# Kernel tuning notes

Hardware: AMD Instinct MI355X
Metric: run time of the kernel (lower is better)

The kernel has to match this reference:

```python
import jax, jax.numpy as jnp
import numpy as np

D = 768      # num_hiddens (hardcoded by dense1/dense2/ln in the source)
H = 12       # num_heads
NEG = -1000000.0
EPS = 1e-5


def setup_inputs() -> dict:
    key = jax.random.key(0)
    ks = jax.random.split(key, 14)
    B, Lq, Lk = 8, 1024, 1024
    s = 0.02
    return {
        "queries": jax.random.normal(ks[0], (B, Lq, D), dtype=jnp.float32),
        "keys":    jax.random.normal(ks[1], (B, Lk, D), dtype=jnp.float32),
        "values":  jax.random.normal(ks[2], (B, Lk, D), dtype=jnp.float32),
        # binary padding masks; count_nonzero along axis 1 gives valid lens
        "mask_1": jax.random.randint(ks[3], (B, Lk), 0, 2, dtype=jnp.int32),
        "mask_2": jax.random.randint(ks[4], (B, Lq), 0, 2, dtype=jnp.int32),
        # projection weights stored as [in, out] (torch Linear is y = x @ W.T)
        "Wq": jax.random.normal(ks[5], (D, D), dtype=jnp.float32) * s,
        "Wk": jax.random.normal(ks[6], (D, D), dtype=jnp.float32) * s,
        "Wv": jax.random.normal(ks[7], (D, D), dtype=jnp.float32) * s,
        "Wo": jax.random.normal(ks[8], (D, D), dtype=jnp.float32) * s,
        "d1_w": jax.random.normal(ks[9], (D, D), dtype=jnp.float32) * s,
        "d1_b": jnp.zeros((D,), dtype=jnp.float32),
        "d2_w": jax.random.normal(ks[10], (D, D), dtype=jnp.float32) * s,
        "d2_b": jnp.zeros((D,), dtype=jnp.float32),
        "ln_g": jnp.ones((D,), dtype=jnp.float32),
        "ln_b": jnp.zeros((D,), dtype=jnp.float32),
    }


def _cross_att(queries, keys, values, mask_1, mask_2,
               Wq, Wk, Wv, Wo, d1_w, d1_b, d2_w, d2_b, ln_g, ln_b):
    B, Lq, _ = queries.shape
    Lk = keys.shape[1]
    hd = D // H
    # project + split heads: [B, H, L, hd]
    q = (queries @ Wq).reshape(B, Lq, H, hd).transpose(0, 2, 1, 3)
    k = (keys    @ Wk).reshape(B, Lk, H, hd).transpose(0, 2, 1, 3)
    v = (values  @ Wv).reshape(B, Lk, H, hd).transpose(0, 2, 1, 3)
    scores = jnp.einsum('bhqd,bhkd->bhqk', q, k) / jnp.sqrt(jnp.float32(hd))
    # dual-axis prefix mask from nonzero counts
    vl1 = jnp.sum(mask_1 != 0, axis=1)  # [B], masks key axis
    vl2 = jnp.sum(mask_2 != 0, axis=1)  # [B], masks query axis
    col_ok = jnp.arange(Lk)[None, None, None, :] < vl1[:, None, None, None]
    row_ok = jnp.arange(Lq)[None, None, :, None] < vl2[:, None, None, None]
    scores = jnp.where(col_ok & row_ok, scores, NEG)
    attn = jax.nn.softmax(scores, axis=-1)
    out = jnp.einsum('bhqk,bhkd->bhqd', attn, v)
    out = out.transpose(0, 2, 1, 3).reshape(B, Lq, D)
    mha = out @ Wo
    ffn = jax.nn.relu(mha @ d1_w + d1_b) @ d2_w + d2_b
    x = ffn + mha  # dropout is identity in eval
    mu = jnp.mean(x, axis=-1, keepdims=True)
    var = jnp.mean(jnp.square(x - mu), axis=-1, keepdims=True)
    return (x - mu) / jnp.sqrt(var + EPS) * ln_g + ln_b


def reference(queries, keys, values, mask_1, mask_2,
              Wq, Wk, Wv, Wo, d1_w, d1_b, d2_w, d2_b, ln_g, ln_b):
    return _cross_att(queries, keys, values, mask_1, mask_2,
                      Wq, Wk, Wv, Wo, d1_w, d1_b, d2_w, d2_b, ln_g, ln_b)
```

## Files before the change

### kernel.cpp

```cpp
#include <hip/hip_runtime.h>
#include <hip/hip_bf16.h>
#include <type_traits>

#define DM   768
#define NH   12
#define HD   64
#define BATCH 8
#define SEQ  1024
#define NROWS (BATCH * SEQ)

typedef short bf16x8 __attribute__((ext_vector_type(8)));
typedef float f32x4 __attribute__((ext_vector_type(4)));

__device__ inline unsigned short f2b(float x) {
    union { float f; unsigned int u; } v; v.f = x;
    return (unsigned short)((v.u + 0x8000u) >> 16);
}
__device__ inline unsigned int f2b2(float lo, float hi) {
    union { float f; unsigned int u; } a, b; a.f = lo; b.f = hi;
    return __builtin_amdgcn_perm(b.u + 0x8000u, a.u + 0x8000u, 0x07060302u);
}
__device__ inline float b2f(unsigned short u) {
    union { float f; unsigned int x; } v; v.x = ((unsigned int)u) << 16;
    return v.f;
}

__device__ inline void gld16(const unsigned short* g, unsigned short* l) {
    __builtin_amdgcn_global_load_lds(
        (const __attribute__((address_space(1))) unsigned int*)g,
        (__attribute__((address_space(3))) unsigned int*)l, 16, 0, 0);
}

__device__ __forceinline__ void mm_loop(const unsigned short* __restrict__ A,
                                        const unsigned short* __restrict__ Wt,
                                        int m0, int n0, int t,
                                        unsigned short (*As)[128][32],
                                        unsigned short (*Ws)[128][32],
                                        f32x4 (&acc)[4][4]) {
    const int w = t >> 6, lane = t & 63;
    const int quad = lane >> 4, l16 = lane & 15;
    const int wm = w & 1, wn = w >> 1;
    const int srow = 16 * w + (lane >> 2);
    const int scol = 8 * ((lane & 3) ^ ((lane >> 3) & 3));
    const int swr = (quad ^ ((l16 >> 1) & 3)) * 8;

#pragma unroll
    for (int i = 0; i < 4; ++i)
#pragma unroll
        for (int j = 0; j < 4; ++j) acc[i][j] = (f32x4){0.f, 0.f, 0.f, 0.f};

    const unsigned short* aP = &A[(size_t)(m0 + srow) * DM + scol];
    const unsigned short* wP = &Wt[(size_t)(n0 + srow) * DM + scol];

    auto stage = [&](int kk, int b) {
#pragma unroll
        for (int j = 0; j < 2; ++j) {
            gld16(aP + (size_t)(64 * j) * DM + kk * 32, &As[b][16 * w + 64 * j][0]);
            gld16(wP + (size_t)(64 * j) * DM + kk * 32, &Ws[b][16 * w + 64 * j][0]);
        }
    };
    auto compute = [&](int b) {
        bf16x8 av[4], bv[4];
#pragma unroll
        for (int i = 0; i < 4; ++i)
            av[i] = *(const bf16x8*)&As[b][wm * 64 + 16 * i + l16][swr];
#pragma unroll
        for (int i = 0; i < 4; ++i)
            bv[i] = *(const bf16x8*)&Ws[b][wn * 64 + 16 * i + l16][swr];
#pragma unroll
        for (int i = 0; i < 4; ++i)
#pragma unroll
            for (int j = 0; j < 4; ++j)
                acc[i][j] = __builtin_amdgcn_mfma_f32_16x16x32_bf16(bv[j], av[i], acc[i][j], 0, 0, 0);
    };

    stage(0, 0);
    stage(1, 1);
    int b = 0;
#pragma unroll 1
    for (int k = 0; k < 22; ++k) {
        int nb = b + 2; if (nb >= 3) nb -= 3;
        stage(k + 2, nb);
        asm volatile("s_waitcnt vmcnt(8)" ::: "memory");
        __builtin_amdgcn_s_barrier();
        compute(b);
        asm volatile("" ::: "memory");
        __builtin_amdgcn_s_barrier();
        if (++b == 3) b = 0;
    }
    asm volatile("s_waitcnt vmcnt(4)" ::: "memory");
    __builtin_amdgcn_s_barrier();
    compute(b);
    asm volatile("" ::: "memory");
    __builtin_amdgcn_s_barrier();
    if (++b == 3) b = 0;
    asm volatile("s_waitcnt vmcnt(0)" ::: "memory");
    __builtin_amdgcn_s_barrier();
    compute(b);
}

__global__ __launch_bounds__(256) void prep_kernel(const float* __restrict__ w0,
                                                   const float* __restrict__ w1,
                                                   const float* __restrict__ w2,
                                                   const float* __restrict__ w3,
                                                   const float* __restrict__ w4,
                                                   const float* __restrict__ w5,
                                                   unsigned short* __restrict__ wt,
                                                   unsigned short* __restrict__ wob,
                                                   const float* __restrict__ qin,
                                                   const float* __restrict__ kin,
                                                   const float* __restrict__ vin,
                                                   unsigned short* __restrict__ oq,
                                                   unsigned short* __restrict__ ok,
                                                   unsigned short* __restrict__ ov) {
    const int z = blockIdx.z;
    const int t = threadIdx.x;

    if (z >= 6) {
        const int linear = (z - 6) * 576 + blockIdx.y * 24 + blockIdx.x;
        const int c0 = linear * 2;
        const int g = c0 / 3072;
        const int r = c0 % 3072;
        const float* src = (g == 0) ? qin : (g == 1) ? kin : vin;
        unsigned short* dst = (g == 0) ? oq : (g == 1) ? ok : ov;
        const size_t i = ((size_t)r * 256 + t) * 8;
        float4 f0 = ((const float4*)(src + i))[0];
        float4 f1 = ((const float4*)(src + i))[1];
        float4 f2 = ((const float4*)(src + i + 2048))[0];
        float4 f3 = ((const float4*)(src + i + 2048))[1];
        uint4 p;
        p.x = f2b2(f0.x, f0.y); p.y = f2b2(f0.z, f0.w);
        p.z = f2b2(f1.x, f1.y); p.w = f2b2(f1.z, f1.w);
        *(uint4*)(dst + i) = p;
        p.x = f2b2(f2.x, f2.y); p.y = f2b2(f2.z, f2.w);
        p.z = f2b2(f3.x, f3.y); p.w = f2b2(f3.z, f3.w);
        *(uint4*)(dst + i + 2048) = p;
        return;
    }

    {
        __shared__ float tile[32][33];
        const float* W = (z == 0) ? w0 : (z == 1) ? w1 : (z == 2) ? w2
                       : (z == 3) ? w3 : (z == 4) ? w4 : w5;
        unsigned short* Wt = wt + (size_t)z * DM * DM;
        const int n0 = blockIdx.x * 32;
        const int k0 = blockIdx.y * 32;
        const int tx = t & 31;
        const int ty = t >> 5;
        float v[4];
#pragma unroll
        for (int r = 0; r < 4; ++r) {
            v[r] = W[(size_t)(k0 + ty + 8 * r) * DM + n0 + tx];
            tile[ty + 8 * r][tx] = v[r];
        }
        if (z == 3) {
#pragma unroll
            for (int r = 0; r < 4; ++r)
                wob[(size_t)(k0 + ty + 8 * r) * DM + n0 + tx] = f2b(v[r]);
        }
        __syncthreads();
#pragma unroll
        for (int r = 0; r < 4; ++r)
            Wt[(size_t)(n0 + ty + 8 * r) * DM + k0 + tx] = f2b(tile[tx][ty + 8 * r]);
    }
}

__global__ __launch_bounds__(256) void qkv_gemm(const unsigned short* __restrict__ aq,
                                                const unsigned short* __restrict__ akk,
                                                const unsigned short* __restrict__ av_,
                                                unsigned short* __restrict__ wt,
                                                const unsigned short* __restrict__ wob,
                                                unsigned short* __restrict__ c0,
                                                unsigned short* __restrict__ c1,
                                                unsigned short* __restrict__ c2,
                                                const int* __restrict__ m1,
                                                const int* __restrict__ m2,
                                                int* __restrict__ lens) {
    __shared__ __align__(16) unsigned short As[3][128][32];
    __shared__ __align__(16) unsigned short Ws[3][128][32];

    const int t = threadIdx.x;
    const size_t WT = (size_t)DM * DM;

    const unsigned short* A;
    const unsigned short* Wop;
    unsigned short* C;
    float cs;
    int m0, n0;

    if (blockIdx.y == 0) {
        if (blockIdx.x >= 52) return;
        if (blockIdx.x >= 36) {
            const int bid = blockIdx.x - 36;
            int* redi = (int*)&As[0][0][0];
            const int b = bid & 7;
            const int* m = (bid < 8) ? m1 : m2;
            int cnt = 0;
            for (int i = t; i < SEQ; i += 256) cnt += (m[b * SEQ + i] != 0) ? 1 : 0;
            redi[t] = cnt;
            __syncthreads();
            for (int off = 128; off > 0; off >>= 1) {
                if (t < off) redi[t] += redi[t + off];
                __syncthreads();
            }
            if (t == 0) lens[bid] = redi[0];
            return;
        }
        A = wt + 4 * WT;
        Wop = wob;
        C = wt + 6 * WT;
        cs = 1.0f;
        m0 = (blockIdx.x % 6) * 128;
        n0 = (blockIdx.x / 6) * 128;
    } else {
        const int yy = blockIdx.y - 1;
        const int g = yy / 6;
        m0 = blockIdx.x * 128;
        n0 = (yy % 6) * 128;
        A = (g == 0) ? aq : (g == 1) ? akk : av_;
        Wop = wt + (size_t)g * WT;
        C = (g == 0) ? c0 : (g == 1) ? c1 : c2;
        cs = (g == 0) ? 0.18033688f : 1.0f;
    }

    f32x4 acc[4][4];
    mm_loop(A, Wop, m0, n0, t, As, Ws, acc);

    const int w = t >> 6, lane = t & 63;
    const int quad = lane >> 4, l16 = lane & 15;
    const int wm = w & 1, wn = w >> 1;

#pragma unroll
    for (int i = 0; i < 4; ++i) {
        const int tok = m0 + wm * 64 + 16 * i + l16;
        unsigned short* crow = &C[(size_t)tok * DM + n0 + wn * 64 + quad * 4];
#pragma unroll
        for (int j = 0; j < 4; ++j) {
            uint2 pr;
            pr.x = f2b2(acc[i][j][0] * cs, acc[i][j][1] * cs);
            pr.y = f2b2(acc[i][j][2] * cs, acc[i][j][3] * cs);
            *(uint2*)(crow + 16 * j) = pr;
        }
    }
}

__global__ __launch_bounds__(256) void vpart_kernel(const unsigned short* __restrict__ v,
                                                    float* __restrict__ vp) {
    __shared__ float red[4][64];
    const int t = threadIdx.x;
    const int bh = blockIdx.x;
    const int chunk = blockIdx.y;
    const int b = bh / NH, h = bh % NH;
    const int d = t & 63, rg = t >> 6;
    const unsigned short* base =
        v + (size_t)(b * SEQ + chunk * 128 + rg * 32) * DM + h * HD + d;
    float s = 0.0f;
#pragma unroll 4
    for (int i = 0; i < 32; ++i) s += b2f(base[(size_t)i * DM]);
    red[rg][d] = s;
    __syncthreads();
    if (rg == 0)
        vp[((size_t)bh * 8 + chunk) * 64 + d] = red[0][d] + red[1][d] + red[2][d] + red[3][d];
}

template <typename CT>
__global__ __launch_bounds__(256) void gemm_bf(const unsigned short* __restrict__ A,
                                               const unsigned short* __restrict__ Wt,
                                               CT* __restrict__ C,
                                               const float* __restrict__ bias,
                                               const unsigned short* __restrict__ res,
                                               int relu) {
    __shared__ __align__(16) unsigned short As[3][128][32];
    __shared__ __align__(16) unsigned short Ws[3][128][32];

    const int t = threadIdx.x;
    const int m0 = blockIdx.x * 128;
    const int n0 = blockIdx.y * 128;

    f32x4 acc[4][4];
    mm_loop(A, Wt, m0, n0, t, As, Ws, acc);

    const int w = t >> 6, lane = t & 63;
    const int quad = lane >> 4, l16 = lane & 15;
    const int wm = w & 1, wn = w >> 1;

#pragma unroll
    for (int i = 0; i < 4; ++i) {
        const int tok = m0 + wm * 64 + 16 * i + l16;
#pragma unroll
        for (int j = 0; j < 4; ++j) {
            const int fb = n0 + wn * 64 + 16 * j + quad * 4;
            float cv0 = acc[i][j][0], cv1 = acc[i][j][1];
            float cv2 = acc[i][j][2], cv3 = acc[i][j][3];
            if (bias) {
                const float4 bb = *(const float4*)&bias[fb];
                cv0 += bb.x; cv1 += bb.y; cv2 += bb.z; cv3 += bb.w;
            }
            if (relu) {
                cv0 = fmaxf(cv0, 0.0f); cv1 = fmaxf(cv1, 0.0f);
                cv2 = fmaxf(cv2, 0.0f); cv3 = fmaxf(cv3, 0.0f);
            }
            if (res) {
                const uint2 rr = *(const uint2*)&res[(size_t)tok * DM + fb];
                cv0 += b2f((unsigned short)(rr.x & 0xffffu));
                cv1 += b2f((unsigned short)(rr.x >> 16));
                cv2 += b2f((unsigned short)(rr.y & 0xffffu));
                cv3 += b2f((unsigned short)(rr.y >> 16));
            }
            if constexpr (std::is_same<CT, float>::value) {
                float4 o4; o4.x = cv0; o4.y = cv1; o4.z = cv2; o4.w = cv3;
                *(float4*)&C[(size_t)tok * DM + fb] = o4;
            } else {
                uint2 pr;
                pr.x = f2b2(cv0, cv1);
                pr.y = f2b2(cv2, cv3);
                *(uint2*)&C[(size_t)tok * DM + fb] = pr;
            }
        }
    }
}

__global__ __launch_bounds__(256) void gemm_mh(const unsigned short* __restrict__ A,
                                               const unsigned short* __restrict__ wt,
                                               unsigned short* __restrict__ cm,
                                               unsigned short* __restrict__ ch,
                                               const float* __restrict__ d1b) {
    __shared__ __align__(16) unsigned short As[3][128][32];
    __shared__ __align__(16) unsigned short Ws[3][128][32];

    const int t = threadIdx.x;
    const int unit = blockIdx.y / 6;
    const unsigned short* Wt = wt + (size_t)(unit ? 6 : 3) * DM * DM;
    unsigned short* C = unit ? ch : cm;
    const int m0 = blockIdx.x * 128;
    const int n0 = (blockIdx.y % 6) * 128;

    f32x4 acc[4][4];
    mm_loop(A, Wt, m0, n0, t, As, Ws, acc);

    const int w = t >> 6, lane = t & 63;
    const int quad = lane >> 4, l16 = lane & 15;
    const int wm = w & 1, wn = w >> 1;

#pragma unroll
    for (int i = 0; i < 4; ++i) {
        const int tok = m0 + wm * 64 + 16 * i + l16;
#pragma unroll
        for (int j = 0; j < 4; ++j) {
            const int fb = n0 + wn * 64 + 16 * j + quad * 4;
            float cv0 = acc[i][j][0], cv1 = acc[i][j][1];
            float cv2 = acc[i][j][2], cv3 = acc[i][j][3];
            if (unit) {
                const float4 bb = *(const float4*)&d1b[fb];
                cv0 = fmaxf(cv0 + bb.x, 0.0f);
                cv1 = fmaxf(cv1 + bb.y, 0.0f);
                cv2 = fmaxf(cv2 + bb.z, 0.0f);
                cv3 = fmaxf(cv3 + bb.w, 0.0f);
            }
            uint2 pr;
            pr.x = f2b2(cv0, cv1);
            pr.y = f2b2(cv2, cv3);
            *(uint2*)&C[(size_t)tok * DM + fb] = pr;
        }
    }
}

__global__ __launch_bounds__(256) void attn_mfma(const unsigned short* Q,
                                                 const unsigned short* __restrict__ K,
                                                 const unsigned short* __restrict__ V,
                                                 unsigned short* O,
                                                 const int* __restrict__ lens,
                                                 const float* __restrict__ vp) {
    __shared__ __align__(16) unsigned short Ks[64][72];
    __shared__ __align__(16) unsigned short Vt[64][72];
    __shared__ __align__(16) unsigned short Ps[4][16][72];

    const int t = threadIdx.x;
    const int bid = blockIdx.x;
    const int q0 = (bid & 15) * 64;
    const int h = (bid >> 4) % NH;
    const int b = bid / (16 * NH);
    const int vl1 = lens[b];
    const int vl2 = lens[8 + b];
    const int wid = t >> 6;
    const int lane = t & 63;
    const int quad = lane >> 4;
    const int l16 = lane & 15;
    const size_t vpb = (size_t)(b * NH + h) * 8 * 64;

    if (q0 >= vl2 || vl1 == 0) {
        float vm[4];
#pragma unroll
        for (int ct = 0; ct < 4; ++ct) {
            float s = 0.0f;
#pragma unroll
            for (int c = 0; c < 8; ++c) s += vp[vpb + (size_t)c * 64 + 16 * ct + l16];
            vm[ct] = s * (1.0f / 1024.0f);
        }
#pragma unroll
        for (int r = 0; r < 4; ++r) {
            const size_t row = (size_t)(b * SEQ + q0 + 16 * wid + quad * 4 + r);
#pragma unroll
            for (int ct = 0; ct < 4; ++ct)
                O[row * DM + h * HD + 16 * ct + l16] = f2b(vm[ct]);
        }
        return;
    }

    bf16x8 qa0, qa1;
    {
        const unsigned short* qp =
            &Q[(size_t)(b * SEQ + q0 + 16 * wid + l16) * DM + h * HD + quad * 8];
        qa0 = *(const bf16x8*)qp;
        qa1 = *(const bf16x8*)(qp + 32);
    }

    f32x4 o[4];
#pragma unroll
    for (int ct = 0; ct < 4; ++ct) o[ct] = (f32x4){0.f, 0.f, 0.f, 0.f};
    float suml[4];
    bool rbad[4];
#pragma unroll
    for (int r = 0; r < 4; ++r) {
        suml[r] = 0.0f;
        rbad[r] = (q0 + 16 * wid + quad * 4 + r) >= vl2;
    }

    const int nt = (vl1 + 63) >> 6;

    const int kkr = t >> 3;
    const int khc = (t & 7) * 8;
    const unsigned short* kbase = &K[(size_t)(b * SEQ) * DM + h * HD];
    const unsigned short* vbase = &V[(size_t)(b * SEQ) * DM + h * HD];

    uint4 kr0 = *(const uint4*)&kbase[(size_t)kkr * DM + khc];
    uint4 kr1 = *(const uint4*)&kbase[(size_t)(kkr + 32) * DM + khc];
    uint4 vr0 = *(const uint4*)&vbase[(size_t)lane * DM + wid * 16];
    uint4 vr1 = *(const uint4*)&vbase[(size_t)lane * DM + wid * 16 + 8];

    const int k2 = l16 >> 2;

    for (int tile = 0; tile < nt; ++tile) {
        const int c0 = tile * 64;
        *(uint4*)&Ks[kkr][khc] = kr0;
        *(uint4*)&Ks[kkr + 32][khc] = kr1;
        {
            union { uint4 u; unsigned short s[8]; } va, vb;
            va.u = vr0; vb.u = vr1;
#pragma unroll
            for (int j = 0; j < 8; ++j) Vt[wid * 16 + j][lane] = va.s[j];
#pragma unroll
            for (int j = 0; j < 8; ++j) Vt[wid * 16 + 8 + j][lane] = vb.s[j];
        }
        __syncthreads();

        if (tile < nt - 1) {
            const int c1 = c0 + 64;
            kr0 = *(const uint4*)&kbase[(size_t)(c1 + kkr) * DM + khc];
            kr1 = *(const uint4*)&kbase[(size_t)(c1 + kkr + 32) * DM + khc];
            vr0 = *(const uint4*)&vbase[(size_t)(c1 + lane) * DM + wid * 16];
            vr1 = *(const uint4*)&vbase[(size_t)(c1 + lane) * DM + wid * 16 + 8];
        }

        f32x4 s[4];
#pragma unroll
        for (int ct = 0; ct < 4; ++ct) {
            f32x4 acc = (f32x4){0.f, 0.f, 0.f, 0.f};
            bf16x8 b0v = *(const bf16x8*)&Ks[16 * ct + l16][quad * 8];
            bf16x8 b1v = *(const bf16x8*)&Ks[16 * ct + l16][32 + quad * 8];
            acc = __builtin_amdgcn_mfma_f32_16x16x32_bf16(qa0, b0v, acc, 0, 0, 0);
            acc = __builtin_amdgcn_mfma_f32_16x16x32_bf16(qa1, b1v, acc, 0, 0, 0);
            s[ct] = acc;
        }
#pragma unroll
        for (int ct = 0; ct < 4; ++ct) {
            const bool kok = (c0 + 16 * ct + l16) < vl1;
#pragma unroll
            for (int r = 0; r < 4; ++r) {
                float e = __builtin_amdgcn_exp2f(s[ct][r]);
                float p = kok ? e : 0.0f;
                s[ct][r] = p;
                suml[r] += p;
            }
        }
#pragma unroll
        for (int ct = 0; ct < 4; ++ct) {
            const int gidx = 2 * ct + (l16 >> 3);
            const int c = l16 & 7;
            const int gs = (gidx ^ quad) * 8 + c;
#pragma unroll
            for (int r = 0; r < 4; ++r)
                Ps[wid][quad * 4 + r][gs] = f2b(s[ct][r]);
        }
        bf16x8 pa0 = *(const bf16x8*)&Ps[wid][l16][(quad ^ k2) * 8];
        bf16x8 pa1 = *(const bf16x8*)&Ps[wid][l16][((4 + quad) ^ k2) * 8];
#pragma unroll
        for (int ct = 0; ct < 4; ++ct) {
            bf16x8 vb0 = *(const bf16x8*)&Vt[16 * ct + l16][quad * 8];
            bf16x8 vb1 = *(const bf16x8*)&Vt[16 * ct + l16][32 + quad * 8];
            o[ct] = __builtin_amdgcn_mfma_f32_16x16x32_bf16(pa0, vb0, o[ct], 0, 0, 0);
            o[ct] = __builtin_amdgcn_mfma_f32_16x16x32_bf16(pa1, vb1, o[ct], 0, 0, 0);
        }
        __syncthreads();
    }

#pragma unroll
    for (int d = 1; d < 16; d <<= 1) {
#pragma unroll
        for (int r = 0; r < 4; ++r) suml[r] += __shfl_xor(suml[r], d, 64);
    }

    float vm[4];
    if (rbad[0] || rbad[3]) {
#pragma unroll
        for (int ct = 0; ct < 4; ++ct) {
            float s = 0.0f;
#pragma unroll
            for (int c = 0; c < 8; ++c) s += vp[vpb + (size_t)c * 64 + 16 * ct + l16];
            vm[ct] = s * (1.0f / 1024.0f);
        }
    }
#pragma unroll
    for (int r = 0; r < 4; ++r) {
        const float inv = 1.0f / suml[r];
        const size_t row = (size_t)(b * SEQ + q0 + 16 * wid + quad * 4 + r);
#pragma unroll
        for (int ct = 0; ct < 4; ++ct) {
            const float val = rbad[r] ? vm[ct] : o[ct][r] * inv;
            O[row * DM + h * HD + 16 * ct + l16] = f2b(val);
        }
    }
}

__global__ __launch_bounds__(256) void ln_kernel(float* __restrict__ X,
                                                 const float* __restrict__ g,
                                                 const float* __restrict__ bvec) {
    __shared__ float red[256];
    const int row = blockIdx.x;
    const int t = threadIdx.x;
    float* xr = X + (size_t)row * DM;
    float x0 = xr[t];
    float x1 = xr[t + 256];
    float x2 = xr[t + 512];
    red[t] = x0 + x1 + x2;
    __syncthreads();
    for (int off = 128; off > 0; off >>= 1) {
        if (t < off) red[t] += red[t + off];
        __syncthreads();
    }
    float mu = red[0] * (1.0f / 768.0f);
    __syncthreads();
    float d0 = x0 - mu, d1 = x1 - mu, d2 = x2 - mu;
    red[t] = d0 * d0 + d1 * d1 + d2 * d2;
    __syncthreads();
    for (int off = 128; off > 0; off >>= 1) {
        if (t < off) red[t] += red[t + off];
        __syncthreads();
    }
    float rstd = rsqrtf(red[0] * (1.0f / 768.0f) + 1e-5f);
    xr[t]       = d0 * rstd * g[t]       + bvec[t];
    xr[t + 256] = d1 * rstd * g[t + 256] + bvec[t + 256];
    xr[t + 512] = d2 * rstd * g[t + 512] + bvec[t + 512];
}

extern "C" void kernel_launch(void* const* d_in, const int* in_sizes, int n_in,
                              void* d_out, int out_size, void* d_ws, size_t ws_size,
                              hipStream_t stream) {
    const float* queries = (const float*)d_in[0];
    const float* keys    = (const float*)d_in[1];
    const float* values  = (const float*)d_in[2];
    const int* mask1 = (const int*)d_in[3];
    const int* mask2 = (const int*)d_in[4];
    const float* Wq  = (const float*)d_in[5];
    const float* Wk  = (const float*)d_in[6];
    const float* Wv  = (const float*)d_in[7];
    const float* Wo  = (const float*)d_in[8];
    const float* d1w = (const float*)d_in[9];
    const float* d1b = (const float*)d_in[10];
    const float* d2w = (const float*)d_in[11];
    const float* d2b = (const float*)d_in[12];
    const float* lng = (const float*)d_in[13];
    const float* lnb = (const float*)d_in[14];

    char* ws = (char*)d_ws;
    int* lens = (int*)ws;
    float* vp = (float*)(ws + 256);
    const size_t VP = (size_t)96 * 8 * 64 * sizeof(float);
    const size_t NB = (size_t)NROWS * DM * sizeof(unsigned short);
    const size_t WT = (size_t)DM * DM;
    unsigned short* b0 = (unsigned short*)(ws + 256 + VP);
    unsigned short* b1 = (unsigned short*)(ws + 256 + VP + NB);
    unsigned short* b2 = (unsigned short*)(ws + 256 + VP + 2 * NB);
    unsigned short* wt = (unsigned short*)(ws + 256 + VP + 3 * NB);
    unsigned short* aq = (unsigned short*)(ws + 256 + VP + 3 * NB + 7 * WT * sizeof(unsigned short));
    unsigned short* ak = aq + (size_t)NROWS * DM;
    unsigned short* av = ak + (size_t)NROWS * DM;
    unsigned short* wob = av + (size_t)NROWS * DM;
    float* xout = (float*)d_out;

    prep_kernel<<<dim3(24, 24, 14), 256, 0, stream>>>(Wq, Wk, Wv, Wo, d1w, d2w,
                                                      wt, wob, queries, keys, values,
                                                      aq, ak, av);

    qkv_gemm<<<dim3(64, 19), 256, 0, stream>>>(aq, ak, av, wt, wob, b0, b1, b2,
                                               mask1, mask2, lens);

    vpart_kernel<<<dim3(96, 8), 256, 0, stream>>>(b2, vp);

    attn_mfma<<<16 * NH * BATCH, 256, 0, stream>>>(b0, b1, b2, b0, lens, vp);

    gemm_mh<<<dim3(64, 12), 256, 0, stream>>>(b0, wt, b1, b2, d1b);

    gemm_bf<float><<<dim3(64, 6), 256, 0, stream>>>(b2, wt + 5 * WT, xout, d2b, b1, 0);

    ln_kernel<<<NROWS, 256, 0, stream>>>(xout, lng, lnb);
}
```

Measured before the change: 311.6 us.

## Fuse fp32-to-bf16 activation conversion into QKV GEMM and use double-buffered loop

Drops the separate pass that converted queries, keys and values to bf16. The QKV GEMM now loads the fp32 activations directly through registers, converts them and writes the bf16 result to LDS, which removes a full write-and-read of the bf16 copies. The shared GEMM main loop also changes from a 3-stage async global_load_lds pipeline with explicit vmcnt waits to a simpler 2-buffer loop using __syncthreads. That lowers LDS use but may expose more load latency in every GEMM. The fused path doubles the global bytes read for A and puts the conversion on the critical path.

```diff
diff --git a/kernel.cpp b/kernel.cpp
--- a/kernel.cpp
+++ b/kernel.cpp
@@ -31,12 +31,14 @@
         (__attribute__((address_space(3))) unsigned int*)l, 16, 0, 0);
 }
 
-__device__ __forceinline__ void mm_loop(const unsigned short* __restrict__ A,
-                                        const unsigned short* __restrict__ Wt,
-                                        int m0, int n0, int t,
-                                        unsigned short (*As)[128][32],
-                                        unsigned short (*Ws)[128][32],
-                                        f32x4 (&acc)[4][4]) {
+template <bool CVT>
+__device__ __forceinline__ void mm_loop2(const unsigned short* __restrict__ A,
+                                         const float* __restrict__ Af,
+                                         const unsigned short* __restrict__ Wt,
+                                         int m0, int n0, int t,
+                                         unsigned short (*As)[128][32],
+                                         unsigned short (*Ws)[128][32],
+                                         f32x4 (&acc)[4][4]) {
     const int w = t >> 6, lane = t & 63;
     const int quad = lane >> 4, l16 = lane & 15;
     const int wm = w & 1, wn = w >> 1;
@@ -49,15 +51,36 @@
 #pragma unroll
         for (int j = 0; j < 4; ++j) acc[i][j] = (f32x4){0.f, 0.f, 0.f, 0.f};
 
-    const unsigned short* aP = &A[(size_t)(m0 + srow) * DM + scol];
-    const unsigned short* wP = &Wt[(size_t)(n0 + srow) * DM + scol];
-
-    auto stage = [&](int kk, int b) {
+    float4 fa[2][2];
+
+    auto loadAf = [&](int k0) {
 #pragma unroll
         for (int j = 0; j < 2; ++j) {
-            gld16(aP + (size_t)(64 * j) * DM + kk * 32, &As[b][16 * w + 64 * j][0]);
-            gld16(wP + (size_t)(64 * j) * DM + kk * 32, &Ws[b][16 * w + 64 * j][0]);
-        }
+            const float* s = &Af[(size_t)(m0 + srow + 64 * j) * DM + k0 + scol];
+            fa[j][0] = ((const float4*)s)[0];
+            fa[j][1] = ((const float4*)s)[1];
+        }
+    };
+    auto writeAf = [&](int b) {
+#pragma unroll
+        for (int j = 0; j < 2; ++j) {
+            uint4 p;
+            p.x = f2b2(fa[j][0].x, fa[j][0].y); p.y = f2b2(fa[j][0].z, fa[j][0].w);
+            p.z = f2b2(fa[j][1].x, fa[j][1].y); p.w = f2b2(fa[j][1].z, fa[j][1].w);
+            *(uint4*)&As[b][srow + 64 * j][(lane & 3) * 8] = p;
+        }
+    };
+    auto stageA = [&](int k0, int b) {
+#pragma unroll
+        for (int j = 0; j < 2; ++j)
+            gld16(&A[(size_t)(m0 + srow + 64 * j) * DM + k0 + scol],
+                  &As[b][16 * w + 64 * j][0]);
+    };
+    auto stageW = [&](int k0, int b) {
+#pragma unroll
+        for (int j = 0; j < 2; ++j)
+            gld16(&Wt[(size_t)(n0 + srow + 64 * j) * DM + k0 + scol],
+                  &Ws[b][16 * w + 64 * j][0]);
     };
     auto compute = [&](int b) {
         bf16x8 av[4], bv[4];
@@ -74,29 +97,21 @@
                 acc[i][j] = __builtin_amdgcn_mfma_f32_16x16x32_bf16(bv[j], av[i], acc[i][j], 0, 0, 0);
     };
 
-    stage(0, 0);
-    stage(1, 1);
-    int b = 0;
-#pragma unroll 1
-    for (int k = 0; k < 22; ++k) {
-        int nb = b + 2; if (nb >= 3) nb -= 3;
-        stage(k + 2, nb);
-        asm volatile("s_waitcnt vmcnt(8)" ::: "memory");
-        __builtin_amdgcn_s_barrier();
-        compute(b);
-        asm volatile("" ::: "memory");
-        __builtin_amdgcn_s_barrier();
-        if (++b == 3) b = 0;
-    }
-    asm volatile("s_waitcnt vmcnt(4)" ::: "memory");
-    __builtin_amdgcn_s_barrier();
-    compute(b);
-    asm volatile("" ::: "memory");
-    __builtin_amdgcn_s_barrier();
-    if (++b == 3) b = 0;
-    asm volatile("s_waitcnt vmcnt(0)" ::: "memory");
-    __builtin_amdgcn_s_barrier();
-    compute(b);
+    if constexpr (CVT) { loadAf(0); writeAf(0); } else { stageA(0, 0); }
+    stageW(0, 0);
+    __syncthreads();
+
+    for (int k0 = 0; k0 < DM; k0 += 32) {
+        const int cur = (k0 >> 5) & 1;
+        if (k0 + 32 < DM) {
+            if constexpr (CVT) loadAf(k0 + 32);
+            else stageA(k0 + 32, cur ^ 1);
+            stageW(k0 + 32, cur ^ 1);
+        }
+        compute(cur);
+        if constexpr (CVT) { if (k0 + 32 < DM) writeAf(cur ^ 1); }
+        __syncthreads();
+    }
 }
 
 __global__ __launch_bounds__(256) void prep_kernel(const float* __restrict__ w0,
@@ -106,68 +121,37 @@
                                                    const float* __restrict__ w4,
                                                    const float* __restrict__ w5,
                                                    unsigned short* __restrict__ wt,
-                                                   unsigned short* __restrict__ wob,
-                                                   const float* __restrict__ qin,
-                                                   const float* __restrict__ kin,
-                                                   const float* __restrict__ vin,
-                                                   unsigned short* __restrict__ oq,
-                                                   unsigned short* __restrict__ ok,
-                                                   unsigned short* __restrict__ ov) {
+                                                   unsigned short* __restrict__ wob) {
     const int z = blockIdx.z;
     const int t = threadIdx.x;
-
-    if (z >= 6) {
-        const int linear = (z - 6) * 576 + blockIdx.y * 24 + blockIdx.x;
-        const int c0 = linear * 2;
-        const int g = c0 / 3072;
-        const int r = c0 % 3072;
-        const float* src = (g == 0) ? qin : (g == 1) ? kin : vin;
-        unsigned short* dst = (g == 0) ? oq : (g == 1) ? ok : ov;
-        const size_t i = ((size_t)r * 256 + t) * 8;
-        float4 f0 = ((const float4*)(src + i))[0];
-        float4 f1 = ((const float4*)(src + i))[1];
-        float4 f2 = ((const float4*)(src + i + 2048))[0];
-        float4 f3 = ((const float4*)(src + i + 2048))[1];
-        uint4 p;
-        p.x = f2b2(f0.x, f0.y); p.y = f2b2(f0.z, f0.w);
-        p.z = f2b2(f1.x, f1.y); p.w = f2b2(f1.z, f1.w);
-        *(uint4*)(dst + i) = p;
-        p.x = f2b2(f2.x, f2.y); p.y = f2b2(f2.z, f2.w);
-        p.z = f2b2(f3.x, f3.y); p.w = f2b2(f3.z, f3.w);
-        *(uint4*)(dst + i + 2048) = p;
-        return;
-    }
-
-    {
-        __shared__ float tile[32][33];
-        const float* W = (z == 0) ? w0 : (z == 1) ? w1 : (z == 2) ? w2
-                       : (z == 3) ? w3 : (z == 4) ? w4 : w5;
-        unsigned short* Wt = wt + (size_t)z * DM * DM;
-        const int n0 = blockIdx.x * 32;
-        const int k0 = blockIdx.y * 32;
-        const int tx = t & 31;
-        const int ty = t >> 5;
-        float v[4];
-#pragma unroll
-        for (int r = 0; r < 4; ++r) {
-            v[r] = W[(size_t)(k0 + ty + 8 * r) * DM + n0 + tx];
-            tile[ty + 8 * r][tx] = v[r];
-        }
-        if (z == 3) {
-#pragma unroll
-            for (int r = 0; r < 4; ++r)
-                wob[(size_t)(k0 + ty + 8 * r) * DM + n0 + tx] = f2b(v[r]);
-        }
-        __syncthreads();
+    __shared__ float tile[32][33];
+    const float* W = (z == 0) ? w0 : (z == 1) ? w1 : (z == 2) ? w2
+                   : (z == 3) ? w3 : (z == 4) ? w4 : w5;
+    unsigned short* Wt = wt + (size_t)z * DM * DM;
+    const int n0 = blockIdx.x * 32;
+    const int k0 = blockIdx.y * 32;
+    const int tx = t & 31;
+    const int ty = t >> 5;
+    float v[4];
+#pragma unroll
+    for (int r = 0; r < 4; ++r) {
+        v[r] = W[(size_t)(k0 + ty + 8 * r) * DM + n0 + tx];
+        tile[ty + 8 * r][tx] = v[r];
+    }
+    if (z == 3) {
 #pragma unroll
         for (int r = 0; r < 4; ++r)
-            Wt[(size_t)(n0 + ty + 8 * r) * DM + k0 + tx] = f2b(tile[tx][ty + 8 * r]);
-    }
-}
-
-__global__ __launch_bounds__(256) void qkv_gemm(const unsigned short* __restrict__ aq,
-                                                const unsigned short* __restrict__ akk,
-                                                const unsigned short* __restrict__ av_,
+            wob[(size_t)(k0 + ty + 8 * r) * DM + n0 + tx] = f2b(v[r]);
+    }
+    __syncthreads();
+#pragma unroll
+    for (int r = 0; r < 4; ++r)
+        Wt[(size_t)(n0 + ty + 8 * r) * DM + k0 + tx] = f2b(tile[tx][ty + 8 * r]);
+}
+
+__global__ __launch_bounds__(256) void qkv_gemm(const float* __restrict__ qin,
+                                                const float* __restrict__ kin,
+                                                const float* __restrict__ vin,
                                                 unsigned short* __restrict__ wt,
                                                 const unsigned short* __restrict__ wob,
                                                 unsigned short* __restrict__ c0,
@@ -176,17 +160,11 @@
                                                 const int* __restrict__ m1,
                                                 const int* __restrict__ m2,
                                                 int* __restrict__ lens) {
-    __shared__ __align__(16) unsigned short As[3][128][32];
-    __shared__ __align__(16) unsigned short Ws[3][128][32];
+    __shared__ __align__(16) unsigned short As[2][128][32];
+    __shared__ __align__(16) unsigned short Ws[2][128][32];
 
     const int t = threadIdx.x;
     const size_t WT = (size_t)DM * DM;
-
-    const unsigned short* A;
-    const unsigned short* Wop;
-    unsigned short* C;
-    float cs;
-    int m0, n0;
 
     if (blockIdx.y == 0) {
         if (blockIdx.x >= 52) return;
@@ -206,25 +184,40 @@
             if (t == 0) lens[bid] = redi[0];
             return;
         }
-        A = wt + 4 * WT;
-        Wop = wob;
-        C = wt + 6 * WT;
-        cs = 1.0f;
-        m0 = (blockIdx.x % 6) * 128;
-        n0 = (blockIdx.x / 6) * 128;
-    } else {
-        const int yy = blockIdx.y - 1;
-        const int g = yy / 6;
-        m0 = blockIdx.x * 128;
-        n0 = (yy % 6) * 128;
-        A = (g == 0) ? aq : (g == 1) ? akk : av_;
-        Wop = wt + (size_t)g * WT;
-        C = (g == 0) ? c0 : (g == 1) ? c1 : c2;
-        cs = (g == 0) ? 0.18033688f : 1.0f;
-    }
+        const int m0 = (blockIdx.x % 6) * 128;
+        const int n0 = (blockIdx.x / 6) * 128;
+        f32x4 acc[4][4];
+        mm_loop2<false>(wt + 4 * WT, nullptr, wob, m0, n0, t, As, Ws, acc);
+        unsigned short* C = wt + 6 * WT;
+        const int w = t >> 6, lane = t & 63;
+        const int quad = lane >> 4, l16 = lane & 15;
+        const int wm = w & 1, wn = w >> 1;
+#pragma unroll
+        for (int i = 0; i < 4; ++i) {
+            const int tok = m0 + wm * 64 + 16 * i + l16;
+            unsigned short* crow = &C[(size_t)tok * DM + n0 + wn * 64 + quad * 4];
+#pragma unroll
+            for (int j = 0; j < 4; ++j) {
+                uint2 pr;
+                pr.x = f2b2(acc[i][j][0], acc[i][j][1]);
+                pr.y = f2b2(acc[i][j][2], acc[i][j][3]);
+                *(uint2*)(crow + 16 * j) = pr;
+            }
+        }
+        return;
+    }
+
+    const int yy = blockIdx.y - 1;
+    const int g = yy / 6;
+    const int m0 = blockIdx.x * 128;
+    const int n0 = (yy % 6) * 128;
+    const float* Af = (g == 0) ? qin : (g == 1) ? kin : vin;
+    const unsigned short* Wop = wt + (size_t)g * WT;
+    unsigned short* C = (g == 0) ? c0 : (g == 1) ? c1 : c2;
+    const float cs = (g == 0) ? 0.18033688f : 1.0f;
 
     f32x4 acc[4][4];
-    mm_loop(A, Wop, m0, n0, t, As, Ws, acc);
+    mm_loop2<true>(nullptr, Af, Wop, m0, n0, t, As, Ws, acc);
 
     const int w = t >> 6, lane = t & 63;
     const int quad = lane >> 4, l16 = lane & 15;
@@ -270,15 +263,15 @@
                                                const float* __restrict__ bias,
                                                const unsigned short* __restrict__ res,
                                                int relu) {
-    __shared__ __align__(16) unsigned short As[3][128][32];
-    __shared__ __align__(16) unsigned short Ws[3][128][32];
+    __shared__ __align__(16) unsigned short As[2][128][32];
+    __shared__ __align__(16) unsigned short Ws[2][128][32];
 
     const int t = threadIdx.x;
     const int m0 = blockIdx.x * 128;
     const int n0 = blockIdx.y * 128;
 
     f32x4 acc[4][4];
-    mm_loop(A, Wt, m0, n0, t, As, Ws, acc);
+    mm_loop2<false>(A, nullptr, Wt, m0, n0, t, As, Ws, acc);
 
     const int w = t >> 6, lane = t & 63;
     const int quad = lane >> 4, l16 = lane & 15;
@@ -325,8 +318,8 @@
                                                unsigned short* __restrict__ cm,
                                                unsigned short* __restrict__ ch,
                                                const float* __restrict__ d1b) {
-    __shared__ __align__(16) unsigned short As[3][128][32];
-    __shared__ __align__(16) unsigned short Ws[3][128][32];
+    __shared__ __align__(16) unsigned short As[2][128][32];
+    __shared__ __align__(16) unsigned short Ws[2][128][32];
 
     const int t = threadIdx.x;
     const int unit = blockIdx.y / 6;
@@ -336,7 +329,7 @@
     const int n0 = (blockIdx.y % 6) * 128;
 
     f32x4 acc[4][4];
-    mm_loop(A, Wt, m0, n0, t, As, Ws, acc);
+    mm_loop2<false>(A, nullptr, Wt, m0, n0, t, As, Ws, acc);
 
     const int w = t >> 6, lane = t & 63;
     const int quad = lane >> 4, l16 = lane & 15;
@@ -592,18 +585,14 @@
     unsigned short* b1 = (unsigned short*)(ws + 256 + VP + NB);
     unsigned short* b2 = (unsigned short*)(ws + 256 + VP + 2 * NB);
     unsigned short* wt = (unsigned short*)(ws + 256 + VP + 3 * NB);
-    unsigned short* aq = (unsigned short*)(ws + 256 + VP + 3 * NB + 7 * WT * sizeof(unsigned short));
-    unsigned short* ak = aq + (size_t)NROWS * DM;
-    unsigned short* av = ak + (size_t)NROWS * DM;
-    unsigned short* wob = av + (size_t)NROWS * DM;
+    unsigned short* wob = wt + 7 * WT;
     float* xout = (float*)d_out;
 
-    prep_kernel<<<dim3(24, 24, 14), 256, 0, stream>>>(Wq, Wk, Wv, Wo, d1w, d2w,
-                                                      wt, wob, queries, keys, values,
-                                                      aq, ak, av);
-
-    qkv_gemm<<<dim3(64, 19), 256, 0, stream>>>(aq, ak, av, wt, wob, b0, b1, b2,
-                                               mask1, mask2, lens);
+    prep_kernel<<<dim3(24, 24, 6), 256, 0, stream>>>(Wq, Wk, Wv, Wo, d1w, d2w,
+                                                     wt, wob);
+
+    qkv_gemm<<<dim3(64, 19), 256, 0, stream>>>(queries, keys, values, wt, wob,
+                                               b0, b1, b2, mask1, mask2, lens);
 
     vpart_kernel<<<dim3(96, 8), 256, 0, stream>>>(b2, vp);
 
```

New measurement: 327.6 us. +5.1%, slower.
